# Kernel tuning notes

Hardware: AMD Instinct MI355X
Metric: run time of the kernel (lower is better)

## Reference

```python
import jax, jax.numpy as jnp
import numpy as np

N_NODES = 100000
N_EDGES = 3200000
N_FEAT = 512
N_HID = 16
N_CLS = 7


def setup_inputs() -> dict:
    key = jax.random.key(0)
    k0, k1, k2, k3 = jax.random.split(key, 4)
    x = jax.random.normal(k0, (N_NODES, N_FEAT), dtype=jnp.float32)
    edge_index = jax.random.randint(k1, (2, N_EDGES), 0, N_NODES, dtype=jnp.int64)
    W1 = jax.random.normal(k2, (N_FEAT, N_HID), dtype=jnp.float32) * (1.0 / np.sqrt(N_FEAT))
    b1 = jnp.zeros((N_HID,), dtype=jnp.float32)
    W2 = jax.random.normal(k3, (N_HID, N_CLS), dtype=jnp.float32) * (1.0 / np.sqrt(N_HID))
    b2 = jnp.zeros((N_CLS,), dtype=jnp.float32)
    return {"x": x, "edge_index": edge_index, "W1": W1, "b1": b1, "W2": W2, "b2": b2}


def _graph_conv(x, src, dst, W, b, n_nodes):
    # transform-then-aggregate: keeps the gathered edge tensor at hidden width
    h = x @ W                                      # [N, out]
    agg = jax.ops.segment_sum(h[src], dst, num_segments=n_nodes)  # [N, out]
    return agg + b


def reference(x, edge_index, W1, b1, W2, b2):
    src, dst = edge_index[0], edge_index[1]
    h = jax.nn.relu(_graph_conv(x, src, dst, W1, b1, N_NODES))
    # dropout is identity in eval mode
    out = _graph_conv(h, src, dst, W2, b2, N_NODES)
    return jax.nn.log_softmax(out, axis=1)
```

## Files before the change

kernel.cpp:

```cpp
#include <hip/hip_runtime.h>

#define NN 100000
#define NE 3200000
#define NF 512
#define NH 16
#define NC 7

#define NB   1024
#define SPAN 98
#define NBLK 256
#define EPB  (NE / NBLK)

__global__ __launch_bounds__(256) void gemm1_kernel(const float* __restrict__ x,
                                                    const float* __restrict__ W1,
                                                    float* __restrict__ h0) {
  const int lane = threadIdx.x & 63;
  const int wave = (blockIdx.x * blockDim.x + threadIdx.x) >> 6;
  const int nwaves = (gridDim.x * blockDim.x) >> 6;

  float w[8][NH];
#pragma unroll
  for (int i = 0; i < 4; ++i) {
#pragma unroll
    for (int j = 0; j < NH; ++j) {
      w[i][j]     = W1[(4 * lane + i) * NH + j];
      w[4 + i][j] = W1[(256 + 4 * lane + i) * NH + j];
    }
  }

  for (int row = wave; row < NN; row += nwaves) {
    const float4* xr = (const float4*)(x + (size_t)row * NF);
    float4 a0 = xr[lane];
    float4 a1 = xr[64 + lane];
    float a[8] = {a0.x, a0.y, a0.z, a0.w, a1.x, a1.y, a1.z, a1.w};

    float acc[NH];
#pragma unroll
    for (int j = 0; j < NH; ++j) acc[j] = 0.f;
#pragma unroll
    for (int i = 0; i < 8; ++i) {
#pragma unroll
      for (int j = 0; j < NH; ++j) acc[j] += a[i] * w[i][j];
    }

    float outv = 0.f;
#pragma unroll
    for (int j = 0; j < NH; ++j) {
      float v = acc[j];
      v += __shfl_xor(v, 1);
      v += __shfl_xor(v, 2);
      v += __shfl_xor(v, 4);
      v += __shfl_xor(v, 8);
      v += __shfl_xor(v, 16);
      v += __shfl_xor(v, 32);
      if (lane == j) outv = v;
    }
    if (lane < NH) h0[(size_t)row * NH + lane] = outv;
  }
}

__global__ __launch_bounds__(512) void countK(const int* __restrict__ ei,
                                              int* __restrict__ bucketCount,
                                              int* __restrict__ blockBase) {
  __shared__ int cnt[NB];
  const int b = blockIdx.x, tid = threadIdx.x;
  for (int i = tid; i < NB; i += 512) cnt[i] = 0;
  __syncthreads();
  const int base = b * EPB;
  for (int e = tid; e < EPB; e += 512) {
    int d = ei[NE + base + e];
    atomicAdd(&cnt[d / SPAN], 1);
  }
  __syncthreads();
  for (int i = tid; i < NB; i += 512) {
    int c = cnt[i];
    blockBase[b * NB + i] = c ? atomicAdd(&bucketCount[i], c) : 0;
  }
}

__global__ __launch_bounds__(1024) void scanK(const int* __restrict__ bucketCount,
                                              int* __restrict__ bucketOffs) {
  __shared__ int sm[NB];
  const int t = threadIdx.x;
  int v = bucketCount[t];
  sm[t] = v;
  __syncthreads();
  for (int off = 1; off < NB; off <<= 1) {
    int u = (t >= off) ? sm[t - off] : 0;
    __syncthreads();
    sm[t] += u;
    __syncthreads();
  }
  bucketOffs[t] = sm[t] - v;
  if (t == NB - 1) bucketOffs[NB] = NE;
}

__global__ __launch_bounds__(512) void scatK(const int* __restrict__ ei,
                                             const int* __restrict__ bucketOffs,
                                             const int* __restrict__ blockBase,
                                             unsigned* __restrict__ pairs) {
  __shared__ int cur[NB];
  const int b = blockIdx.x, tid = threadIdx.x;
  for (int i = tid; i < NB; i += 512) cur[i] = 0;
  __syncthreads();
  const int base = b * EPB;
  for (int e = tid; e < EPB; e += 512) {
    int s = ei[base + e];
    int d = ei[NE + base + e];
    int j = d / SPAN;
    int dl = d - j * SPAN;
    int r = atomicAdd(&cur[j], 1);
    pairs[bucketOffs[j] + blockBase[b * NB + j] + r] = (unsigned)s | ((unsigned)dl << 17);
  }
}

__global__ __launch_bounds__(512) void agg16K(const int* __restrict__ bucketOffs,
                                              const unsigned* __restrict__ pairs,
                                              const float* __restrict__ h0,
                                              float* __restrict__ agg) {
  __shared__ float acc[SPAN * NH];
  const int j = blockIdx.x, tid = threadIdx.x;
  for (int i = tid; i < SPAN * NH; i += 512) acc[i] = 0.f;
  __syncthreads();
  const int beg = bucketOffs[j], end = bucketOffs[j + 1];
  const int col = tid & 15, slot = tid >> 4;
  int e = beg + slot;
  for (; e + 96 < end; e += 128) {
    unsigned pk0 = pairs[e];
    unsigned pk1 = pairs[e + 32];
    unsigned pk2 = pairs[e + 64];
    unsigned pk3 = pairs[e + 96];
    float v0 = h0[(size_t)(pk0 & 0x1FFFF) * NH + col];
    float v1 = h0[(size_t)(pk1 & 0x1FFFF) * NH + col];
    float v2 = h0[(size_t)(pk2 & 0x1FFFF) * NH + col];
    float v3 = h0[(size_t)(pk3 & 0x1FFFF) * NH + col];
    atomicAdd(&acc[(pk0 >> 17) * NH + col], v0);
    atomicAdd(&acc[(pk1 >> 17) * NH + col], v1);
    atomicAdd(&acc[(pk2 >> 17) * NH + col], v2);
    atomicAdd(&acc[(pk3 >> 17) * NH + col], v3);
  }
  for (; e < end; e += 32) {
    unsigned pk = pairs[e];
    atomicAdd(&acc[(pk >> 17) * NH + col], h0[(size_t)(pk & 0x1FFFF) * NH + col]);
  }
  __syncthreads();
  const int lo = j * SPAN;
  for (int i = tid; i < SPAN * NH; i += 512) {
    int node = lo + (i >> 4);
    if (node < NN) agg[(size_t)node * NH + (i & 15)] = acc[i];
  }
}

__global__ __launch_bounds__(256) void transform_kernel(const float* __restrict__ agg1,
                                                        const float* __restrict__ b1,
                                                        const float* __restrict__ W2,
                                                        float* __restrict__ p) {
  int n = blockIdx.x * blockDim.x + threadIdx.x;
  if (n >= NN) return;
  const float4* r = (const float4*)(agg1 + (size_t)n * NH);
  float4 v0 = r[0], v1 = r[1], v2 = r[2], v3 = r[3];
  float h[NH] = {v0.x, v0.y, v0.z, v0.w, v1.x, v1.y, v1.z, v1.w,
                 v2.x, v2.y, v2.z, v2.w, v3.x, v3.y, v3.z, v3.w};
#pragma unroll
  for (int k = 0; k < NH; ++k) h[k] = fmaxf(h[k] + b1[k], 0.f);

#pragma unroll
  for (int j = 0; j < NC; ++j) {
    float acc = 0.f;
#pragma unroll
    for (int k = 0; k < NH; ++k) acc += h[k] * W2[k * NC + j];
    p[(size_t)n * 8 + j] = acc;
  }
  p[(size_t)n * 8 + 7] = 0.f;
}

__global__ __launch_bounds__(512) void agg8K(const int* __restrict__ bucketOffs,
                                             const unsigned* __restrict__ pairs,
                                             const float* __restrict__ p,
                                             float* __restrict__ agg) {
  __shared__ float acc[SPAN * 8];
  const int j = blockIdx.x, tid = threadIdx.x;
  for (int i = tid; i < SPAN * 8; i += 512) acc[i] = 0.f;
  __syncthreads();
  const int beg = bucketOffs[j], end = bucketOffs[j + 1];
  const int col = tid & 7, slot = tid >> 3;
  int e = beg + slot;
  for (; e + 192 < end; e += 256) {
    unsigned pk0 = pairs[e];
    unsigned pk1 = pairs[e + 64];
    unsigned pk2 = pairs[e + 128];
    unsigned pk3 = pairs[e + 192];
    float v0 = p[(size_t)(pk0 & 0x1FFFF) * 8 + col];
    float v1 = p[(size_t)(pk1 & 0x1FFFF) * 8 + col];
    float v2 = p[(size_t)(pk2 & 0x1FFFF) * 8 + col];
    float v3 = p[(size_t)(pk3 & 0x1FFFF) * 8 + col];
    atomicAdd(&acc[(pk0 >> 17) * 8 + col], v0);
    atomicAdd(&acc[(pk1 >> 17) * 8 + col], v1);
    atomicAdd(&acc[(pk2 >> 17) * 8 + col], v2);
    atomicAdd(&acc[(pk3 >> 17) * 8 + col], v3);
  }
  for (; e < end; e += 64) {
    unsigned pk = pairs[e];
    atomicAdd(&acc[(pk >> 17) * 8 + col], p[(size_t)(pk & 0x1FFFF) * 8 + col]);
  }
  __syncthreads();
  const int lo = j * SPAN;
  for (int i = tid; i < SPAN * 8; i += 512) {
    int node = lo + (i >> 3);
    if (node < NN) agg[(size_t)node * 8 + (i & 7)] = acc[i];
  }
}

__global__ __launch_bounds__(256) void lsm_kernel(const float* __restrict__ agg2,
                                                  const float* __restrict__ b2,
                                                  float* __restrict__ out) {
  int n = blockIdx.x * blockDim.x + threadIdx.x;
  if (n >= NN) return;
  float z[NC];
  float m = -1e30f;
#pragma unroll
  for (int j = 0; j < NC; ++j) {
    z[j] = agg2[(size_t)n * 8 + j] + b2[j];
    m = fmaxf(m, z[j]);
  }
  float s = 0.f;
#pragma unroll
  for (int j = 0; j < NC; ++j) s += __expf(z[j] - m);
  float l = __logf(s);
#pragma unroll
  for (int j = 0; j < NC; ++j) out[(size_t)n * NC + j] = z[j] - m - l;
}

__global__ __launch_bounds__(256) void scatter16_kernel(const int* __restrict__ ei,
                                                        const float* __restrict__ h0,
                                                        float* __restrict__ agg) {
  long long gid = (long long)blockIdx.x * blockDim.x + threadIdx.x;
  int e = (int)(gid >> 4);
  if (e >= NE) return;
  int j = (int)(gid & 15);
  int s = ei[e];
  int d = ei[NE + e];
  atomicAdd(&agg[(size_t)d * NH + j], h0[(size_t)s * NH + j]);
}

__global__ __launch_bounds__(256) void scatter7_kernel(const int* __restrict__ ei,
                                                       const float* __restrict__ p,
                                                       float* __restrict__ agg) {
  long long gid = (long long)blockIdx.x * blockDim.x + threadIdx.x;
  int e = (int)(gid >> 3);
  if (e >= NE) return;
  int j = (int)(gid & 7);
  if (j >= NC) return;
  int s = ei[e];
  int d = ei[NE + e];
  atomicAdd(&agg[(size_t)d * 8 + j], p[(size_t)s * 8 + j]);
}

extern "C" void kernel_launch(void* const* d_in, const int* in_sizes, int n_in,
                              void* d_out, int out_size, void* d_ws, size_t ws_size,
                              hipStream_t stream) {
  const float* x  = (const float*)d_in[0];
  const int*   ei = (const int*)d_in[1];
  const float* W1 = (const float*)d_in[2];
  const float* b1 = (const float*)d_in[3];
  const float* W2 = (const float*)d_in[4];
  const float* b2 = (const float*)d_in[5];
  float* out = (float*)d_out;

  float*    h0p  = (float*)d_ws;
  float*    aggp = h0p + (size_t)NN * NH;
  unsigned* pairs = (unsigned*)(aggp + (size_t)NN * NH);
  int* bucketCount = (int*)(pairs + NE);
  int* bucketOffs  = bucketCount + NB;
  int* blockBase   = (int*)aggp;
  size_t need = (size_t)((char*)(bucketOffs + NB + 1) - (char*)d_ws);

  if (ws_size >= need) {
    hipMemsetAsync(bucketCount, 0, NB * sizeof(int), stream);
    countK<<<NBLK, 512, 0, stream>>>(ei, bucketCount, blockBase);
    scanK<<<1, NB, 0, stream>>>(bucketCount, bucketOffs);
    scatK<<<NBLK, 512, 0, stream>>>(ei, bucketOffs, blockBase, pairs);

    gemm1_kernel<<<2048, 256, 0, stream>>>(x, W1, h0p);
    agg16K<<<NB, 512, 0, stream>>>(bucketOffs, pairs, h0p, aggp);
    transform_kernel<<<(NN + 255) / 256, 256, 0, stream>>>(aggp, b1, W2, h0p);
    agg8K<<<NB, 512, 0, stream>>>(bucketOffs, pairs, h0p, aggp);
    lsm_kernel<<<(NN + 255) / 256, 256, 0, stream>>>(aggp, b2, out);
  } else {
    float* bufA = (float*)d_ws;
    float* bufB = bufA + (size_t)NN * NH;

    hipMemsetAsync(bufB, 0, (size_t)NN * NH * sizeof(float), stream);
    gemm1_kernel<<<2048, 256, 0, stream>>>(x, W1, bufA);
    scatter16_kernel<<<(int)(((long long)NE * 16 + 255) / 256), 256, 0, stream>>>(ei, bufA, bufB);
    transform_kernel<<<(NN + 255) / 256, 256, 0, stream>>>(bufB, b1, W2, bufA);
    hipMemsetAsync(bufB, 0, (size_t)NN * 8 * sizeof(float), stream);
    scatter7_kernel<<<(int)(((long long)NE * 8 + 255) / 256), 256, 0, stream>>>(ei, bufA, bufB);
    lsm_kernel<<<(NN + 255) / 256, 256, 0, stream>>>(bufB, b2, out);
  }
}
```

Before: 846.1 us.

## Split each bucket's aggregation across multiple blocks with atomic global flush

Each destination bucket is now processed by KSPL=8 blocks instead of one, with each block taking an interleaved slice of the bucket's edges. Every block accumulates into its own shared-memory tile, then atomically adds the nonzero entries into global agg, which is zeroed by new memsets beforehand. The aim is more parallelism and latency hiding, since 1024 blocks of about 3125 edges each may underfill the GPU. The cost is eight times the shared-memory init and flush work, global atomics, and two extra memsets.

```diff
diff --git a/kernel.cpp b/kernel.cpp
--- a/kernel.cpp
+++ b/kernel.cpp
@@ -8,6 +8,7 @@
 
 #define NB   1024
 #define SPAN 98
+#define KSPL 8
 #define NBLK 256
 #define EPB  (NE / NBLK)
 
@@ -119,17 +120,20 @@
                                               const float* __restrict__ h0,
                                               float* __restrict__ agg) {
   __shared__ float acc[SPAN * NH];
-  const int j = blockIdx.x, tid = threadIdx.x;
+  const int j = blockIdx.x >> 3;
+  const int k = blockIdx.x & (KSPL - 1);
+  const int tid = threadIdx.x;
   for (int i = tid; i < SPAN * NH; i += 512) acc[i] = 0.f;
   __syncthreads();
   const int beg = bucketOffs[j], end = bucketOffs[j + 1];
-  const int col = tid & 15, slot = tid >> 4;
+  const int col = tid & 15;
+  const int slot = k * 32 + (tid >> 4);
   int e = beg + slot;
-  for (; e + 96 < end; e += 128) {
+  for (; e + 3 * 256 < end; e += 4 * 256) {
     unsigned pk0 = pairs[e];
-    unsigned pk1 = pairs[e + 32];
-    unsigned pk2 = pairs[e + 64];
-    unsigned pk3 = pairs[e + 96];
+    unsigned pk1 = pairs[e + 256];
+    unsigned pk2 = pairs[e + 512];
+    unsigned pk3 = pairs[e + 768];
     float v0 = h0[(size_t)(pk0 & 0x1FFFF) * NH + col];
     float v1 = h0[(size_t)(pk1 & 0x1FFFF) * NH + col];
     float v2 = h0[(size_t)(pk2 & 0x1FFFF) * NH + col];
@@ -139,7 +143,7 @@
     atomicAdd(&acc[(pk2 >> 17) * NH + col], v2);
     atomicAdd(&acc[(pk3 >> 17) * NH + col], v3);
   }
-  for (; e < end; e += 32) {
+  for (; e < end; e += 256) {
     unsigned pk = pairs[e];
     atomicAdd(&acc[(pk >> 17) * NH + col], h0[(size_t)(pk & 0x1FFFF) * NH + col]);
   }
@@ -147,7 +151,8 @@
   const int lo = j * SPAN;
   for (int i = tid; i < SPAN * NH; i += 512) {
     int node = lo + (i >> 4);
-    if (node < NN) agg[(size_t)node * NH + (i & 15)] = acc[i];
+    float v = acc[i];
+    if (node < NN && v != 0.f) atomicAdd(&agg[(size_t)node * NH + (i & 15)], v);
   }
 }
 
@@ -179,17 +184,20 @@
                                              const float* __restrict__ p,
                                              float* __restrict__ agg) {
   __shared__ float acc[SPAN * 8];
-  const int j = blockIdx.x, tid = threadIdx.x;
+  const int j = blockIdx.x >> 3;
+  const int k = blockIdx.x & (KSPL - 1);
+  const int tid = threadIdx.x;
   for (int i = tid; i < SPAN * 8; i += 512) acc[i] = 0.f;
   __syncthreads();
   const int beg = bucketOffs[j], end = bucketOffs[j + 1];
-  const int col = tid & 7, slot = tid >> 3;
+  const int col = tid & 7;
+  const int slot = k * 64 + (tid >> 3);
   int e = beg + slot;
-  for (; e + 192 < end; e += 256) {
+  for (; e + 3 * 512 < end; e += 4 * 512) {
     unsigned pk0 = pairs[e];
-    unsigned pk1 = pairs[e + 64];
-    unsigned pk2 = pairs[e + 128];
-    unsigned pk3 = pairs[e + 192];
+    unsigned pk1 = pairs[e + 512];
+    unsigned pk2 = pairs[e + 1024];
+    unsigned pk3 = pairs[e + 1536];
     float v0 = p[(size_t)(pk0 & 0x1FFFF) * 8 + col];
     float v1 = p[(size_t)(pk1 & 0x1FFFF) * 8 + col];
     float v2 = p[(size_t)(pk2 & 0x1FFFF) * 8 + col];
@@ -199,7 +207,7 @@
     atomicAdd(&acc[(pk2 >> 17) * 8 + col], v2);
     atomicAdd(&acc[(pk3 >> 17) * 8 + col], v3);
   }
-  for (; e < end; e += 64) {
+  for (; e < end; e += 512) {
     unsigned pk = pairs[e];
     atomicAdd(&acc[(pk >> 17) * 8 + col], p[(size_t)(pk & 0x1FFFF) * 8 + col]);
   }
@@ -207,7 +215,8 @@
   const int lo = j * SPAN;
   for (int i = tid; i < SPAN * 8; i += 512) {
     int node = lo + (i >> 3);
-    if (node < NN) agg[(size_t)node * 8 + (i & 7)] = acc[i];
+    float v = acc[i];
+    if (node < NN && v != 0.f) atomicAdd(&agg[(size_t)node * 8 + (i & 7)], v);
   }
 }
 
@@ -282,9 +291,11 @@
     scatK<<<NBLK, 512, 0, stream>>>(ei, bucketOffs, blockBase, pairs);
 
     gemm1_kernel<<<2048, 256, 0, stream>>>(x, W1, h0p);
-    agg16K<<<NB, 512, 0, stream>>>(bucketOffs, pairs, h0p, aggp);
+    hipMemsetAsync(aggp, 0, (size_t)NN * NH * sizeof(float), stream);
+    agg16K<<<NB * KSPL, 512, 0, stream>>>(bucketOffs, pairs, h0p, aggp);
     transform_kernel<<<(NN + 255) / 256, 256, 0, stream>>>(aggp, b1, W2, h0p);
-    agg8K<<<NB, 512, 0, stream>>>(bucketOffs, pairs, h0p, aggp);
+    hipMemsetAsync(aggp, 0, (size_t)NN * 8 * sizeof(float), stream);
+    agg8K<<<NB * KSPL, 512, 0, stream>>>(bucketOffs, pairs, h0p, aggp);
     lsm_kernel<<<(NN + 255) / 256, 256, 0, stream>>>(aggp, b2, out);
   } else {
     float* bufA = (float*)d_ws;
```

Measured after the change: 883.8 us. 4.5% more time.
